# Optimization experiments

Hardware: AMD Instinct MI355X
Metric: run time of the kernel (lower is better)

Reference implementation:

```python
import jax, jax.numpy as jnp
import numpy as np

N_NODES = 100000
N_EDGES = 1600000
D_IN = 128
D_OUT = 128


def setup_inputs() -> dict:
    key = jax.random.key(0)
    k1, k2, k3, k4, k5, k6 = jax.random.split(key, 6)
    x = jax.random.normal(k1, (N_NODES, D_IN), dtype=jnp.float32)
    row = jnp.sort(jax.random.randint(k2, (N_EDGES,), 0, N_NODES, dtype=jnp.int32))
    col = jax.random.randint(k3, (N_EDGES,), 0, N_NODES, dtype=jnp.int32)
    val = jax.random.uniform(k4, (N_EDGES,), dtype=jnp.float32)
    # Glorot init for the two linear weights (stored as [in, out] for x @ W)
    std_l = float(np.sqrt(6.0 / (D_IN + D_OUT)))
    W_l = jax.random.uniform(k5, (D_IN, D_OUT), minval=-std_l, maxval=std_l, dtype=jnp.float32)
    b_l = jnp.zeros((D_OUT,), dtype=jnp.float32)
    W_r = jax.random.uniform(k6, (D_IN, D_OUT), minval=-std_l, maxval=std_l, dtype=jnp.float32)
    return {"x": x, "row": row, "col": col, "val": val, "W_l": W_l, "b_l": b_l, "W_r": W_r}


def reference(x, row, col, val, W_l, b_l, W_r):
    n = x.shape[0]
    # out_l = graph @ x  (sparse COO matmul: gather source feats, scale, scatter-add to rows)
    msg = val[:, None] * x[col]                      # [E, D_in]
    out_l = jax.ops.segment_sum(msg, row, num_segments=n)  # [N, D_in]
    # lin_l(out_l) + lin_r(x)
    return out_l @ W_l + b_l + x @ W_r
```

## Files before the change

### kernel.cpp

```cpp
#include <hip/hip_runtime.h>

#define D 128
#define EDGE_CAP 1024
typedef unsigned int uint32;
typedef __bf16 bf16x8 __attribute__((ext_vector_type(8)));
typedef float f32x4 __attribute__((ext_vector_type(4)));

__device__ __forceinline__ unsigned short f2bf(float f) {
    unsigned u = __float_as_uint(f);
    unsigned r = u + 0x7FFFu + ((u >> 16) & 1u);
    return (unsigned short)(r >> 16);
}
__device__ __forceinline__ float bflo(uint32 u) { return __uint_as_float(u << 16); }
__device__ __forceinline__ float bfhi(uint32 u) { return __uint_as_float(u & 0xFFFF0000u); }

__device__ __forceinline__ void fma8(float* acc, uint4 r, float v) {
    acc[0] += v * bflo(r.x); acc[1] += v * bfhi(r.x);
    acc[2] += v * bflo(r.y); acc[3] += v * bfhi(r.y);
    acc[4] += v * bflo(r.z); acc[5] += v * bfhi(r.z);
    acc[6] += v * bflo(r.w); acc[7] += v * bfhi(r.w);
}

__global__ __launch_bounds__(256) void prep_kernel(
    const float* __restrict__ x, unsigned short* __restrict__ xh, int n8,
    const int* __restrict__ row, int* __restrict__ row_ptr,
    int n_nodes, int n_edges,
    const float* __restrict__ Wl, const float* __restrict__ Wr,
    unsigned short* __restrict__ Wlt, unsigned short* __restrict__ Wrt,
    int nbConv, int nbRp) {
    const int b = blockIdx.x;
    if (b < nbConv) {
        const int id = b * 256 + threadIdx.x;
        if (id < n8) {
            const float4* p = (const float4*)x + (size_t)id * 2;
            float4 a = p[0], bb = p[1];
            uint4 o;
            o.x = f2bf(a.x) | ((uint32)f2bf(a.y) << 16);
            o.y = f2bf(a.z) | ((uint32)f2bf(a.w) << 16);
            o.z = f2bf(bb.x) | ((uint32)f2bf(bb.y) << 16);
            o.w = f2bf(bb.z) | ((uint32)f2bf(bb.w) << 16);
            ((uint4*)xh)[id] = o;
        }
    } else if (b < nbConv + nbRp) {
        const int e = (b - nbConv) * 256 + threadIdx.x;
        if (e < n_edges) {
            const int r = row[e];
            const int rp = (e == 0) ? -1 : row[e - 1];
            for (int n = rp + 1; n <= r; ++n) row_ptr[n] = e;
            if (e == n_edges - 1)
                for (int n = r + 1; n <= n_nodes; ++n) row_ptr[n] = n_edges;
        }
    } else {
        const int id = (b - nbConv - nbRp) * 256 + threadIdx.x;
        if (id < 16384) {
            const int n = id & 127, k = id >> 7;
            Wlt[n * 128 + k] = f2bf(Wl[k * 128 + n]);
            Wrt[n * 128 + k] = f2bf(Wr[k * 128 + n]);
        }
    }
}

__global__ __launch_bounds__(256) void spmm_gemm_kernel(
    const unsigned short* __restrict__ xh,
    const int* __restrict__ row_ptr,
    const int* __restrict__ col,
    const float* __restrict__ val,
    const unsigned short* __restrict__ Wlt,
    const unsigned short* __restrict__ Wrt,
    const float* __restrict__ b_l,
    float* __restrict__ out, int n_nodes) {
    __shared__ int2 scv[EDGE_CAP];
    __shared__ unsigned short A_lds[16][264];
    const int tid = threadIdx.x;
    const int n0 = blockIdx.x * 16;
    const int e0 = row_ptr[n0];
    const int e1 = row_ptr[min(n0 + 16, n_nodes)];
    const int ne = e1 - e0;
    const bool fits = (ne <= EDGE_CAP);
    if (fits) {
        for (int t = tid; t < ne; t += 256)
            scv[t] = make_int2(col[e0 + t], __float_as_int(val[e0 + t]));
    }

    {
        const int r = tid >> 4, ch = tid & 15;
        uint4 v = make_uint4(0u, 0u, 0u, 0u);
        if (n0 + r < n_nodes)
            v = *(const uint4*)&xh[(size_t)(n0 + r) * D + ch * 8];
        *(uint4*)&A_lds[r][128 + ch * 8] = v;
    }
    __syncthreads();

    const int wv = tid >> 6, lane = tid & 63;
    const int g = lane >> 4, lq = lane & 15;
    const int nloc = wv * 4 + g;
    const int n = n0 + nloc;

    int s = 0, e = 0;
    if (n < n_nodes) { s = row_ptr[n]; e = row_ptr[n + 1]; }

    float acc[8] = {0.f, 0.f, 0.f, 0.f, 0.f, 0.f, 0.f, 0.f};

    if (fits) {
        auto fetch = [&](int idx, int& c, float& v) {
            if (idx < e) {
                const int li = idx - e0;
                if (li < EDGE_CAP) { c = scv[li].x; v = __int_as_float(scv[li].y); }
                else               { c = col[idx]; v = val[idx]; }
            } else { c = 0; v = 0.f; }
        };

        int i = s;
        int c0, c1, c2, c3; float v0, v1, v2, v3;
        fetch(i + 0, c0, v0); fetch(i + 1, c1, v1);
        fetch(i + 2, c2, v2); fetch(i + 3, c3, v3);
        uint4 r0 = *(const uint4*)&xh[c0 * D + lq * 8];
        uint4 r1 = *(const uint4*)&xh[c1 * D + lq * 8];
        uint4 r2 = *(const uint4*)&xh[c2 * D + lq * 8];
        uint4 r3 = *(const uint4*)&xh[c3 * D + lq * 8];

        while (i < e) {
            const int i2 = i + 4;
            int d0, d1, d2, d3; float w0, w1, w2, w3;
            fetch(i2 + 0, d0, w0); fetch(i2 + 1, d1, w1);
            fetch(i2 + 2, d2, w2); fetch(i2 + 3, d3, w3);
            const uint4 t0 = *(const uint4*)&xh[d0 * D + lq * 8];
            const uint4 t1 = *(const uint4*)&xh[d1 * D + lq * 8];
            const uint4 t2 = *(const uint4*)&xh[d2 * D + lq * 8];
            const uint4 t3 = *(const uint4*)&xh[d3 * D + lq * 8];
            fma8(acc, r0, v0);
            fma8(acc, r1, v1);
            fma8(acc, r2, v2);
            fma8(acc, r3, v3);
            r0 = t0; r1 = t1; r2 = t2; r3 = t3;
            v0 = w0; v1 = w1; v2 = w2; v3 = w3;
            i = i2;
        }
    } else {
        for (int j = s; j < e; ++j) {
            const int c = col[j];
            const float v = val[j];
            const uint4 r = *(const uint4*)&xh[(size_t)c * D + lq * 8];
            fma8(acc, r, v);
        }
    }

    {
        uint4 o;
        o.x = f2bf(acc[0]) | ((uint32)f2bf(acc[1]) << 16);
        o.y = f2bf(acc[2]) | ((uint32)f2bf(acc[3]) << 16);
        o.z = f2bf(acc[4]) | ((uint32)f2bf(acc[5]) << 16);
        o.w = f2bf(acc[6]) | ((uint32)f2bf(acc[7]) << 16);
        *(uint4*)&A_lds[nloc][lq * 8] = o;
    }
    __syncthreads();

    const int fr = lane & 15;
    const int kofs = (lane >> 4) * 8;
    f32x4 acc2[2];
    acc2[0] = (f32x4){0.f, 0.f, 0.f, 0.f};
    acc2[1] = (f32x4){0.f, 0.f, 0.f, 0.f};
#pragma unroll
    for (int st = 0; st < 8; ++st) {
        const int k0 = st * 32;
        const unsigned short* Wsel = (k0 < 128) ? Wlt : Wrt;
        const int kk = k0 & 127;
        const bf16x8 a = *(const bf16x8*)&A_lds[fr][k0 + kofs];
#pragma unroll
        for (int nr = 0; nr < 2; ++nr) {
            const int ncol = wv * 32 + nr * 16 + fr;
            const bf16x8 b = *(const bf16x8*)&Wsel[ncol * 128 + kk + kofs];
            acc2[nr] = __builtin_amdgcn_mfma_f32_16x16x32_bf16(
                a, b, acc2[nr], 0, 0, 0);
        }
    }
    const int r0c = (lane >> 4) * 4;
#pragma unroll
    for (int nr = 0; nr < 2; ++nr) {
        const int ncol = wv * 32 + nr * 16 + fr;
        const float bias = b_l[ncol];
#pragma unroll
        for (int j = 0; j < 4; ++j) {
            const int m = n0 + r0c + j;
            if (m < n_nodes) out[(size_t)m * D + ncol] = acc2[nr][j] + bias;
        }
    }
}

__global__ void build_rowptr_kernel(const int* __restrict__ row,
                                    int* __restrict__ row_ptr,
                                    int n_nodes, int n_edges) {
    int e = blockIdx.x * blockDim.x + threadIdx.x;
    if (e >= n_edges) return;
    int r = row[e];
    int rp = (e == 0) ? -1 : row[e - 1];
    for (int n = rp + 1; n <= r; ++n) row_ptr[n] = e;
    if (e == n_edges - 1)
        for (int n = r + 1; n <= n_nodes; ++n) row_ptr[n] = n_edges;
}

__global__ __launch_bounds__(128) void spmm_kernel(
    const float* __restrict__ x, const int* __restrict__ row_ptr,
    const int* __restrict__ col, const float* __restrict__ val,
    float* __restrict__ out_l) {
    const int n = blockIdx.x;
    const int d = threadIdx.x;
    const int start = row_ptr[n];
    const int end = row_ptr[n + 1];
    float acc = 0.0f;
    for (int e = start; e < end; ++e)
        acc += val[e] * x[(size_t)col[e] * D + d];
    out_l[(size_t)n * D + d] = acc;
}

__global__ __launch_bounds__(256) void fused_gemm_kernel(
    const float* __restrict__ xin, const float* __restrict__ W_l,
    const float* __restrict__ b_l, const float* __restrict__ W_r,
    float* __restrict__ out, int M) {
    __shared__ float As[64][68];
    __shared__ float Ws[64][132];
    const int tid = threadIdx.x;
    const int tx = tid & 15;
    const int ty = tid >> 4;
    const int ty4 = ty * 4;
    const int m0 = blockIdx.x * 64;
    float acc[4][8];
#pragma unroll
    for (int i = 0; i < 4; ++i)
#pragma unroll
        for (int j = 0; j < 8; ++j) acc[i][j] = 0.0f;
    for (int kt = 0; kt < 4; ++kt) {
        const float* Asrc = (kt < 2) ? out : xin;
        const float* Wsrc = (kt < 2) ? W_l : W_r;
        const int koff = (kt & 1) * 64;
        __syncthreads();
#pragma unroll
        for (int r = 0; r < 4; ++r) {
            const int idx = tid + r * 256;
            const int m = idx >> 4;
            const int kq = idx & 15;
            float4 a = make_float4(0.f, 0.f, 0.f, 0.f);
            if (m0 + m < M)
                a = *(const float4*)&Asrc[(size_t)(m0 + m) * D + koff + kq * 4];
            *(float4*)&As[m][kq * 4] = a;
        }
#pragma unroll
        for (int r = 0; r < 8; ++r) {
            const int idx = tid + r * 256;
            const int k = idx >> 5;
            const int j4 = idx & 31;
            *(float4*)&Ws[k][j4 * 4] =
                *(const float4*)&Wsrc[(size_t)(koff + k) * D + j4 * 4];
        }
        __syncthreads();
#pragma unroll 4
        for (int k = 0; k < 64; ++k) {
            const float a0 = As[ty4 + 0][k], a1 = As[ty4 + 1][k];
            const float a2 = As[ty4 + 2][k], a3 = As[ty4 + 3][k];
            const float4 w0 = *(const float4*)&Ws[k][tx * 4];
            const float4 w1 = *(const float4*)&Ws[k][64 + tx * 4];
            acc[0][0] += a0 * w0.x; acc[0][1] += a0 * w0.y; acc[0][2] += a0 * w0.z; acc[0][3] += a0 * w0.w;
            acc[0][4] += a0 * w1.x; acc[0][5] += a0 * w1.y; acc[0][6] += a0 * w1.z; acc[0][7] += a0 * w1.w;
            acc[1][0] += a1 * w0.x; acc[1][1] += a1 * w0.y; acc[1][2] += a1 * w0.z; acc[1][3] += a1 * w0.w;
            acc[1][4] += a1 * w1.x; acc[1][5] += a1 * w1.y; acc[1][6] += a1 * w1.z; acc[1][7] += a1 * w1.w;
            acc[2][0] += a2 * w0.x; acc[2][1] += a2 * w0.y; acc[2][2] += a2 * w0.z; acc[2][3] += a2 * w0.w;
            acc[2][4] += a2 * w1.x; acc[2][5] += a2 * w1.y; acc[2][6] += a2 * w1.z; acc[2][7] += a2 * w1.w;
            acc[3][0] += a3 * w0.x; acc[3][1] += a3 * w0.y; acc[3][2] += a3 * w0.z; acc[3][3] += a3 * w0.w;
            acc[3][4] += a3 * w1.x; acc[3][5] += a3 * w1.y; acc[3][6] += a3 * w1.z; acc[3][7] += a3 * w1.w;
        }
    }
    const float4 bv0 = *(const float4*)&b_l[tx * 4];
    const float4 bv1 = *(const float4*)&b_l[64 + tx * 4];
#pragma unroll
    for (int i = 0; i < 4; ++i) {
        const int m = m0 + ty4 + i;
        if (m < M) {
            float4 o0, o1;
            o0.x = acc[i][0] + bv0.x; o0.y = acc[i][1] + bv0.y;
            o0.z = acc[i][2] + bv0.z; o0.w = acc[i][3] + bv0.w;
            o1.x = acc[i][4] + bv1.x; o1.y = acc[i][5] + bv1.y;
            o1.z = acc[i][6] + bv1.z; o1.w = acc[i][7] + bv1.w;
            *(float4*)&out[(size_t)m * D + tx * 4] = o0;
            *(float4*)&out[(size_t)m * D + 64 + tx * 4] = o1;
        }
    }
}

static inline size_t align256(size_t x) { return (x + 255) & ~(size_t)255; }

extern "C" void kernel_launch(void* const* d_in, const int* in_sizes, int n_in,
                              void* d_out, int out_size, void* d_ws, size_t ws_size,
                              hipStream_t stream) {
    const float* x   = (const float*)d_in[0];
    const int*   row = (const int*)d_in[1];
    const int*   col = (const int*)d_in[2];
    const float* val = (const float*)d_in[3];
    const float* W_l = (const float*)d_in[4];
    const float* b_l = (const float*)d_in[5];
    const float* W_r = (const float*)d_in[6];
    float* out = (float*)d_out;

    const int n_nodes = in_sizes[0] / D;
    const int n_edges = in_sizes[1];

    const size_t xh_bytes = (size_t)n_nodes * D * 2;
    const size_t wt_bytes = (size_t)D * D * 2;
    const size_t rp_bytes = (size_t)(n_nodes + 1) * 4;
    size_t off = 0;
    const size_t xh_off  = off; off += align256(xh_bytes);
    const size_t wlt_off = off; off += align256(wt_bytes);
    const size_t wrt_off = off; off += align256(wt_bytes);
    const size_t rp_off  = off; off += align256(rp_bytes);
    const size_t needed  = off + 65536;

    if (ws_size >= needed) {
        unsigned short* xh  = (unsigned short*)((char*)d_ws + xh_off);
        unsigned short* Wlt = (unsigned short*)((char*)d_ws + wlt_off);
        unsigned short* Wrt = (unsigned short*)((char*)d_ws + wrt_off);
        int* row_ptr        = (int*)((char*)d_ws + rp_off);

        const int n8 = n_nodes * D / 8;
        const int nbConv = (n8 + 255) / 256;
        const int nbRp   = (n_edges + 255) / 256;
        const int nbW    = 64;
        prep_kernel<<<nbConv + nbRp + nbW, 256, 0, stream>>>(
            x, xh, n8, row, row_ptr, n_nodes, n_edges,
            W_l, W_r, Wlt, Wrt, nbConv, nbRp);
        spmm_gemm_kernel<<<(n_nodes + 15) / 16, 256, 0, stream>>>(
            xh, row_ptr, col, val, Wlt, Wrt, b_l, out, n_nodes);
    } else {
        int* row_ptr = (int*)d_ws;
        build_rowptr_kernel<<<(n_edges + 255) / 256, 256, 0, stream>>>(
            row, row_ptr, n_nodes, n_edges);
        spmm_kernel<<<n_nodes, 128, 0, stream>>>(x, row_ptr, col, val, out);
        fused_gemm_kernel<<<(n_nodes + 63) / 64, 256, 0, stream>>>(
            x, W_l, b_l, W_r, out, n_nodes);
    }
}
```

Before: 108.9 us.

## Process 64 nodes per block with per-wave 16-row tiles and full-width MFMA

Each block now handles 64 nodes instead of 16, and each wave owns 16 rows end to end. A wave runs the SpMM for its rows (4 rows per lane group), writes them to a swizzled per-wave LDS tile, then computes all 128 output columns with MFMA, reading the x rows for the right-hand term straight from global memory. This drops the second block-wide barrier and cuts per-block overhead by a factor of four. In exchange there are fewer blocks, more serial SpMM work per lane group and larger edge staging (2048), which may lower occupancy and latency hiding.

Measured after the change: 140.8 us. +29.3%, slower.

```diff
diff --git a/kernel.cpp b/kernel.cpp
--- a/kernel.cpp
+++ b/kernel.cpp
@@ -1,7 +1,7 @@
 #include <hip/hip_runtime.h>
 
 #define D 128
-#define EDGE_CAP 1024
+#define ECAP 2048
 typedef unsigned int uint32;
 typedef __bf16 bf16x8 __attribute__((ext_vector_type(8)));
 typedef float f32x4 __attribute__((ext_vector_type(4)));
@@ -69,120 +69,123 @@
     const unsigned short* __restrict__ Wrt,
     const float* __restrict__ b_l,
     float* __restrict__ out, int n_nodes) {
-    __shared__ int2 scv[EDGE_CAP];
-    __shared__ unsigned short A_lds[16][264];
+    __shared__ int2 scv[ECAP];
+    __shared__ unsigned short A_w[4][16][128];
     const int tid = threadIdx.x;
-    const int n0 = blockIdx.x * 16;
-    const int e0 = row_ptr[n0];
-    const int e1 = row_ptr[min(n0 + 16, n_nodes)];
-    const int ne = e1 - e0;
-    const bool fits = (ne <= EDGE_CAP);
+    const int n0 = blockIdx.x * 64;
+    const int E0 = row_ptr[n0];
+    const int E1 = row_ptr[min(n0 + 64, n_nodes)];
+    const int ne = E1 - E0;
+    const bool fits = (ne <= ECAP);
     if (fits) {
         for (int t = tid; t < ne; t += 256)
-            scv[t] = make_int2(col[e0 + t], __float_as_int(val[e0 + t]));
-    }
-
-    {
-        const int r = tid >> 4, ch = tid & 15;
-        uint4 v = make_uint4(0u, 0u, 0u, 0u);
-        if (n0 + r < n_nodes)
-            v = *(const uint4*)&xh[(size_t)(n0 + r) * D + ch * 8];
-        *(uint4*)&A_lds[r][128 + ch * 8] = v;
+            scv[t] = make_int2(col[E0 + t], __float_as_int(val[E0 + t]));
     }
     __syncthreads();
 
     const int wv = tid >> 6, lane = tid & 63;
     const int g = lane >> 4, lq = lane & 15;
-    const int nloc = wv * 4 + g;
-    const int n = n0 + nloc;
-
-    int s = 0, e = 0;
-    if (n < n_nodes) { s = row_ptr[n]; e = row_ptr[n + 1]; }
-
-    float acc[8] = {0.f, 0.f, 0.f, 0.f, 0.f, 0.f, 0.f, 0.f};
-
-    if (fits) {
-        auto fetch = [&](int idx, int& c, float& v) {
-            if (idx < e) {
-                const int li = idx - e0;
-                if (li < EDGE_CAP) { c = scv[li].x; v = __int_as_float(scv[li].y); }
-                else               { c = col[idx]; v = val[idx]; }
-            } else { c = 0; v = 0.f; }
-        };
-
-        int i = s;
-        int c0, c1, c2, c3; float v0, v1, v2, v3;
-        fetch(i + 0, c0, v0); fetch(i + 1, c1, v1);
-        fetch(i + 2, c2, v2); fetch(i + 3, c3, v3);
-        uint4 r0 = *(const uint4*)&xh[c0 * D + lq * 8];
-        uint4 r1 = *(const uint4*)&xh[c1 * D + lq * 8];
-        uint4 r2 = *(const uint4*)&xh[c2 * D + lq * 8];
-        uint4 r3 = *(const uint4*)&xh[c3 * D + lq * 8];
-
-        while (i < e) {
-            const int i2 = i + 4;
-            int d0, d1, d2, d3; float w0, w1, w2, w3;
-            fetch(i2 + 0, d0, w0); fetch(i2 + 1, d1, w1);
-            fetch(i2 + 2, d2, w2); fetch(i2 + 3, d3, w3);
-            const uint4 t0 = *(const uint4*)&xh[d0 * D + lq * 8];
-            const uint4 t1 = *(const uint4*)&xh[d1 * D + lq * 8];
-            const uint4 t2 = *(const uint4*)&xh[d2 * D + lq * 8];
-            const uint4 t3 = *(const uint4*)&xh[d3 * D + lq * 8];
-            fma8(acc, r0, v0);
-            fma8(acc, r1, v1);
-            fma8(acc, r2, v2);
-            fma8(acc, r3, v3);
-            r0 = t0; r1 = t1; r2 = t2; r3 = t3;
-            v0 = w0; v1 = w1; v2 = w2; v3 = w3;
-            i = i2;
-        }
-    } else {
-        for (int j = s; j < e; ++j) {
-            const int c = col[j];
-            const float v = val[j];
-            const uint4 r = *(const uint4*)&xh[(size_t)c * D + lq * 8];
-            fma8(acc, r, v);
-        }
-    }
-
-    {
+    const int nw0 = n0 + wv * 16;
+
+    for (int i = 0; i < 4; ++i) {
+        const int rowl = g * 4 + i;
+        const int node = nw0 + rowl;
+        int s = 0, e = 0;
+        if (node < n_nodes) { s = row_ptr[node]; e = row_ptr[node + 1]; }
+
+        float acc[8] = {0.f, 0.f, 0.f, 0.f, 0.f, 0.f, 0.f, 0.f};
+
+        if (fits) {
+            auto fetch = [&](int idx, int& c, float& v) {
+                if (idx < e) {
+                    const int li = idx - E0;
+                    c = scv[li].x; v = __int_as_float(scv[li].y);
+                } else { c = 0; v = 0.f; }
+            };
+            int ii = s;
+            int c0, c1, c2, c3; float v0, v1, v2, v3;
+            fetch(ii + 0, c0, v0); fetch(ii + 1, c1, v1);
+            fetch(ii + 2, c2, v2); fetch(ii + 3, c3, v3);
+            uint4 r0 = *(const uint4*)&xh[c0 * D + lq * 8];
+            uint4 r1 = *(const uint4*)&xh[c1 * D + lq * 8];
+            uint4 r2 = *(const uint4*)&xh[c2 * D + lq * 8];
+            uint4 r3 = *(const uint4*)&xh[c3 * D + lq * 8];
+            while (ii < e) {
+                const int i2 = ii + 4;
+                int d0, d1, d2, d3; float w0, w1, w2, w3;
+                fetch(i2 + 0, d0, w0); fetch(i2 + 1, d1, w1);
+                fetch(i2 + 2, d2, w2); fetch(i2 + 3, d3, w3);
+                const uint4 t0 = *(const uint4*)&xh[d0 * D + lq * 8];
+                const uint4 t1 = *(const uint4*)&xh[d1 * D + lq * 8];
+                const uint4 t2 = *(const uint4*)&xh[d2 * D + lq * 8];
+                const uint4 t3 = *(const uint4*)&xh[d3 * D + lq * 8];
+                fma8(acc, r0, v0);
+                fma8(acc, r1, v1);
+                fma8(acc, r2, v2);
+                fma8(acc, r3, v3);
+                r0 = t0; r1 = t1; r2 = t2; r3 = t3;
+                v0 = w0; v1 = w1; v2 = w2; v3 = w3;
+                ii = i2;
+            }
+        } else {
+            for (int j = s; j < e; ++j) {
+                const int c = col[j];
+                const float v = val[j];
+                const uint4 r = *(const uint4*)&xh[(size_t)c * D + lq * 8];
+                fma8(acc, r, v);
+            }
+        }
+
         uint4 o;
         o.x = f2bf(acc[0]) | ((uint32)f2bf(acc[1]) << 16);
         o.y = f2bf(acc[2]) | ((uint32)f2bf(acc[3]) << 16);
         o.z = f2bf(acc[4]) | ((uint32)f2bf(acc[5]) << 16);
         o.w = f2bf(acc[6]) | ((uint32)f2bf(acc[7]) << 16);
-        *(uint4*)&A_lds[nloc][lq * 8] = o;
-    }
-    __syncthreads();
-
-    const int fr = lane & 15;
-    const int kofs = (lane >> 4) * 8;
-    f32x4 acc2[2];
-    acc2[0] = (f32x4){0.f, 0.f, 0.f, 0.f};
-    acc2[1] = (f32x4){0.f, 0.f, 0.f, 0.f};
-#pragma unroll
-    for (int st = 0; st < 8; ++st) {
+        const int sidx = (lq * 8) ^ ((rowl & 7) << 3);
+        *(uint4*)&A_w[wv][rowl][sidx] = o;
+    }
+
+    const int fr = lane & 15, hh = lane >> 4;
+    const int kofs = hh * 8;
+    f32x4 acc2[8];
+#pragma unroll
+    for (int nt = 0; nt < 8; ++nt) acc2[nt] = (f32x4){0.f, 0.f, 0.f, 0.f};
+
+#pragma unroll
+    for (int st = 0; st < 4; ++st) {
         const int k0 = st * 32;
-        const unsigned short* Wsel = (k0 < 128) ? Wlt : Wrt;
-        const int kk = k0 & 127;
-        const bf16x8 a = *(const bf16x8*)&A_lds[fr][k0 + kofs];
-#pragma unroll
-        for (int nr = 0; nr < 2; ++nr) {
-            const int ncol = wv * 32 + nr * 16 + fr;
-            const bf16x8 b = *(const bf16x8*)&Wsel[ncol * 128 + kk + kofs];
-            acc2[nr] = __builtin_amdgcn_mfma_f32_16x16x32_bf16(
-                a, b, acc2[nr], 0, 0, 0);
-        }
-    }
-    const int r0c = (lane >> 4) * 4;
-#pragma unroll
-    for (int nr = 0; nr < 2; ++nr) {
-        const int ncol = wv * 32 + nr * 16 + fr;
+        const int aidx = (k0 + kofs) ^ ((fr & 7) << 3);
+        const bf16x8 a = *(const bf16x8*)&A_w[wv][fr][aidx];
+#pragma unroll
+        for (int nt = 0; nt < 8; ++nt) {
+            const bf16x8 b =
+                *(const bf16x8*)&Wlt[(nt * 16 + fr) * 128 + k0 + kofs];
+            acc2[nt] = __builtin_amdgcn_mfma_f32_16x16x32_bf16(
+                a, b, acc2[nt], 0, 0, 0);
+        }
+    }
+#pragma unroll
+    for (int st = 0; st < 4; ++st) {
+        const int k0 = st * 32;
+        const bf16x8 a =
+            *(const bf16x8*)&xh[(size_t)(nw0 + fr) * D + k0 + kofs];
+#pragma unroll
+        for (int nt = 0; nt < 8; ++nt) {
+            const bf16x8 b =
+                *(const bf16x8*)&Wrt[(nt * 16 + fr) * 128 + k0 + kofs];
+            acc2[nt] = __builtin_amdgcn_mfma_f32_16x16x32_bf16(
+                a, b, acc2[nt], 0, 0, 0);
+        }
+    }
+
+#pragma unroll
+    for (int nt = 0; nt < 8; ++nt) {
+        const int ncol = nt * 16 + fr;
         const float bias = b_l[ncol];
 #pragma unroll
         for (int j = 0; j < 4; ++j) {
-            const int m = n0 + r0c + j;
-            if (m < n_nodes) out[(size_t)m * D + ncol] = acc2[nr][j] + bias;
+            const int m = nw0 + hh * 4 + j;
+            if (m < n_nodes) out[(size_t)m * D + ncol] = acc2[nt][j] + bias;
         }
     }
 }
@@ -326,7 +329,7 @@
         prep_kernel<<<nbConv + nbRp + nbW, 256, 0, stream>>>(
             x, xh, n8, row, row_ptr, n_nodes, n_edges,
             W_l, W_r, Wlt, Wrt, nbConv, nbRp);
-        spmm_gemm_kernel<<<(n_nodes + 15) / 16, 256, 0, stream>>>(
+        spmm_gemm_kernel<<<(n_nodes + 63) / 64, 256, 0, stream>>>(
             xh, row_ptr, col, val, Wlt, Wrt, b_l, out, n_nodes);
     } else {
         int* row_ptr = (int*)d_ws;
```

## Process two 16-node tiles per block, overlapping staging with MFMA epilogue

Applied to the files above, without the earlier changes.

Each block now handles 32 nodes as two 16-row tiles with double-buffered LDS. The edge list and x rows for the second tile are staged while the first tile's MFMA epilogue runs, aiming to hide load latency and amortize W loads. LDS rows are XOR-swizzled instead of padded to avoid bank conflicts. The grid is halved, which reduces the number of blocks available for parallelism, and the in-loop fallback to global memory for edges beyond the LDS cap was removed.

Result: slower. 125.2 us (+15.0%).

```diff
diff --git a/kernel.cpp b/kernel.cpp
--- a/kernel.cpp
+++ b/kernel.cpp
@@ -70,120 +70,140 @@
     const float* __restrict__ b_l,
     float* __restrict__ out, int n_nodes) {
     __shared__ int2 scv[EDGE_CAP];
-    __shared__ unsigned short A_lds[16][264];
+    __shared__ unsigned short A[2][16][256];
     const int tid = threadIdx.x;
-    const int n0 = blockIdx.x * 16;
-    const int e0 = row_ptr[n0];
-    const int e1 = row_ptr[min(n0 + 16, n_nodes)];
-    const int ne = e1 - e0;
-    const bool fits = (ne <= EDGE_CAP);
-    if (fits) {
-        for (int t = tid; t < ne; t += 256)
-            scv[t] = make_int2(col[e0 + t], __float_as_int(val[e0 + t]));
-    }
-
-    {
-        const int r = tid >> 4, ch = tid & 15;
+    const int wv = tid >> 6, lane = tid & 63;
+    const int g = lane >> 4, lq = lane & 15;
+
+    const int n0a = blockIdx.x * 32;
+    const int n0b = n0a + 16;
+    const bool haveB = (n0b < n_nodes);
+
+    int e0a = 0, e0b = 0;
+    bool fita = false, fitb = false;
+
+    auto stage_scv = [&](int n0, int& e0, bool& fits) {
+        e0 = row_ptr[n0];
+        const int e1 = row_ptr[min(n0 + 16, n_nodes)];
+        const int ne = e1 - e0;
+        fits = (ne <= EDGE_CAP);
+        if (fits) {
+            for (int t = tid; t < ne; t += 256)
+                scv[t] = make_int2(col[e0 + t], __float_as_int(val[e0 + t]));
+        }
+    };
+    auto stage_x = [&](int buf, int n0) {
+        const int r = tid >> 4, c = tid & 15;
         uint4 v = make_uint4(0u, 0u, 0u, 0u);
         if (n0 + r < n_nodes)
-            v = *(const uint4*)&xh[(size_t)(n0 + r) * D + ch * 8];
-        *(uint4*)&A_lds[r][128 + ch * 8] = v;
-    }
-    __syncthreads();
-
-    const int wv = tid >> 6, lane = tid & 63;
-    const int g = lane >> 4, lq = lane & 15;
-    const int nloc = wv * 4 + g;
-    const int n = n0 + nloc;
-
-    int s = 0, e = 0;
-    if (n < n_nodes) { s = row_ptr[n]; e = row_ptr[n + 1]; }
-
-    float acc[8] = {0.f, 0.f, 0.f, 0.f, 0.f, 0.f, 0.f, 0.f};
-
-    if (fits) {
-        auto fetch = [&](int idx, int& c, float& v) {
-            if (idx < e) {
-                const int li = idx - e0;
-                if (li < EDGE_CAP) { c = scv[li].x; v = __int_as_float(scv[li].y); }
-                else               { c = col[idx]; v = val[idx]; }
-            } else { c = 0; v = 0.f; }
-        };
-
-        int i = s;
-        int c0, c1, c2, c3; float v0, v1, v2, v3;
-        fetch(i + 0, c0, v0); fetch(i + 1, c1, v1);
-        fetch(i + 2, c2, v2); fetch(i + 3, c3, v3);
-        uint4 r0 = *(const uint4*)&xh[c0 * D + lq * 8];
-        uint4 r1 = *(const uint4*)&xh[c1 * D + lq * 8];
-        uint4 r2 = *(const uint4*)&xh[c2 * D + lq * 8];
-        uint4 r3 = *(const uint4*)&xh[c3 * D + lq * 8];
-
-        while (i < e) {
-            const int i2 = i + 4;
-            int d0, d1, d2, d3; float w0, w1, w2, w3;
-            fetch(i2 + 0, d0, w0); fetch(i2 + 1, d1, w1);
-            fetch(i2 + 2, d2, w2); fetch(i2 + 3, d3, w3);
-            const uint4 t0 = *(const uint4*)&xh[d0 * D + lq * 8];
-            const uint4 t1 = *(const uint4*)&xh[d1 * D + lq * 8];
-            const uint4 t2 = *(const uint4*)&xh[d2 * D + lq * 8];
-            const uint4 t3 = *(const uint4*)&xh[d3 * D + lq * 8];
-            fma8(acc, r0, v0);
-            fma8(acc, r1, v1);
-            fma8(acc, r2, v2);
-            fma8(acc, r3, v3);
-            r0 = t0; r1 = t1; r2 = t2; r3 = t3;
-            v0 = w0; v1 = w1; v2 = w2; v3 = w3;
-            i = i2;
-        }
-    } else {
-        for (int j = s; j < e; ++j) {
-            const int c = col[j];
-            const float v = val[j];
-            const uint4 r = *(const uint4*)&xh[(size_t)c * D + lq * 8];
-            fma8(acc, r, v);
-        }
-    }
-
-    {
+            v = *(const uint4*)&xh[(size_t)(n0 + r) * D + c * 8];
+        *(uint4*)&A[buf][r][128 + ((c ^ (r & 7)) * 8)] = v;
+    };
+
+    auto gather = [&](int buf, int n0, int e0, bool fits) {
+        const int nloc = wv * 4 + g;
+        const int n = n0 + nloc;
+        int s = 0, e = 0;
+        if (n < n_nodes) { s = row_ptr[n]; e = row_ptr[n + 1]; }
+        float acc[8] = {0.f, 0.f, 0.f, 0.f, 0.f, 0.f, 0.f, 0.f};
+
+        if (fits) {
+            auto fetch = [&](int idx, int& c, float& v) {
+                if (idx < e) {
+                    const int li = idx - e0;
+                    c = scv[li].x; v = __int_as_float(scv[li].y);
+                } else { c = 0; v = 0.f; }
+            };
+            int i = s;
+            int c0, c1, c2, c3; float v0, v1, v2, v3;
+            fetch(i + 0, c0, v0); fetch(i + 1, c1, v1);
+            fetch(i + 2, c2, v2); fetch(i + 3, c3, v3);
+            uint4 r0 = *(const uint4*)&xh[c0 * D + lq * 8];
+            uint4 r1 = *(const uint4*)&xh[c1 * D + lq * 8];
+            uint4 r2 = *(const uint4*)&xh[c2 * D + lq * 8];
+            uint4 r3 = *(const uint4*)&xh[c3 * D + lq * 8];
+            while (i < e) {
+                const int i2 = i + 4;
+                int d0, d1, d2, d3; float w0, w1, w2, w3;
+                fetch(i2 + 0, d0, w0); fetch(i2 + 1, d1, w1);
+                fetch(i2 + 2, d2, w2); fetch(i2 + 3, d3, w3);
+                const uint4 t0 = *(const uint4*)&xh[d0 * D + lq * 8];
+                const uint4 t1 = *(const uint4*)&xh[d1 * D + lq * 8];
+                const uint4 t2 = *(const uint4*)&xh[d2 * D + lq * 8];
+                const uint4 t3 = *(const uint4*)&xh[d3 * D + lq * 8];
+                fma8(acc, r0, v0);
+                fma8(acc, r1, v1);
+                fma8(acc, r2, v2);
+                fma8(acc, r3, v3);
+                r0 = t0; r1 = t1; r2 = t2; r3 = t3;
+                v0 = w0; v1 = w1; v2 = w2; v3 = w3;
+                i = i2;
+            }
+        } else {
+            for (int j = s; j < e; ++j) {
+                const int c = col[j];
+                const float v = val[j];
+                const uint4 r = *(const uint4*)&xh[(size_t)c * D + lq * 8];
+                fma8(acc, r, v);
+            }
+        }
+
         uint4 o;
         o.x = f2bf(acc[0]) | ((uint32)f2bf(acc[1]) << 16);
         o.y = f2bf(acc[2]) | ((uint32)f2bf(acc[3]) << 16);
         o.z = f2bf(acc[4]) | ((uint32)f2bf(acc[5]) << 16);
         o.w = f2bf(acc[6]) | ((uint32)f2bf(acc[7]) << 16);
-        *(uint4*)&A_lds[nloc][lq * 8] = o;
-    }
-    __syncthreads();
-
-    const int fr = lane & 15;
-    const int kofs = (lane >> 4) * 8;
-    f32x4 acc2[2];
-    acc2[0] = (f32x4){0.f, 0.f, 0.f, 0.f};
-    acc2[1] = (f32x4){0.f, 0.f, 0.f, 0.f};
-#pragma unroll
-    for (int st = 0; st < 8; ++st) {
-        const int k0 = st * 32;
-        const unsigned short* Wsel = (k0 < 128) ? Wlt : Wrt;
-        const int kk = k0 & 127;
-        const bf16x8 a = *(const bf16x8*)&A_lds[fr][k0 + kofs];
+        *(uint4*)&A[buf][nloc][(lq ^ (nloc & 7)) * 8] = o;
+    };
+
+    auto epilogue = [&](int buf, int n0) {
+        const int fr = lane & 15, hh = lane >> 4;
+        const int kofs = hh * 8;
+        f32x4 acc2[2];
+        acc2[0] = (f32x4){0.f, 0.f, 0.f, 0.f};
+        acc2[1] = (f32x4){0.f, 0.f, 0.f, 0.f};
+#pragma unroll
+        for (int st = 0; st < 8; ++st) {
+            const int h = st >> 2;
+            const int cc = (st & 3) * 4 + hh;
+            const bf16x8 a =
+                *(const bf16x8*)&A[buf][fr][h * 128 + ((cc ^ (fr & 7)) * 8)];
+            const unsigned short* Wsel = h ? Wrt : Wlt;
+            const int kk = (st & 3) * 32 + kofs;
+#pragma unroll
+            for (int nr = 0; nr < 2; ++nr) {
+                const int ncol = wv * 32 + nr * 16 + fr;
+                const bf16x8 b = *(const bf16x8*)&Wsel[ncol * 128 + kk];
+                acc2[nr] = __builtin_amdgcn_mfma_f32_16x16x32_bf16(
+                    a, b, acc2[nr], 0, 0, 0);
+            }
+        }
+        const int r0c = hh * 4;
 #pragma unroll
         for (int nr = 0; nr < 2; ++nr) {
             const int ncol = wv * 32 + nr * 16 + fr;
-            const bf16x8 b = *(const bf16x8*)&Wsel[ncol * 128 + kk + kofs];
-            acc2[nr] = __builtin_amdgcn_mfma_f32_16x16x32_bf16(
-                a, b, acc2[nr], 0, 0, 0);
-        }
-    }
-    const int r0c = (lane >> 4) * 4;
-#pragma unroll
-    for (int nr = 0; nr < 2; ++nr) {
-        const int ncol = wv * 32 + nr * 16 + fr;
-        const float bias = b_l[ncol];
-#pragma unroll
-        for (int j = 0; j < 4; ++j) {
-            const int m = n0 + r0c + j;
-            if (m < n_nodes) out[(size_t)m * D + ncol] = acc2[nr][j] + bias;
-        }
+            const float bias = b_l[ncol];
+#pragma unroll
+            for (int j = 0; j < 4; ++j) {
+                const int m = n0 + r0c + j;
+                if (m < n_nodes)
+                    out[(size_t)m * D + ncol] = acc2[nr][j] + bias;
+            }
+        }
+    };
+
+    stage_scv(n0a, e0a, fita);
+    stage_x(0, n0a);
+    __syncthreads();
+    gather(0, n0a, e0a, fita);
+    __syncthreads();
+    if (haveB) { stage_scv(n0b, e0b, fitb); stage_x(1, n0b); }
+    epilogue(0, n0a);
+    __syncthreads();
+    if (haveB) {
+        gather(1, n0b, e0b, fitb);
+        __syncthreads();
+        epilogue(1, n0b);
     }
 }
 
@@ -326,7 +346,7 @@
         prep_kernel<<<nbConv + nbRp + nbW, 256, 0, stream>>>(
             x, xh, n8, row, row_ptr, n_nodes, n_edges,
             W_l, W_r, Wlt, Wrt, nbConv, nbRp);
-        spmm_gemm_kernel<<<(n_nodes + 15) / 16, 256, 0, stream>>>(
+        spmm_gemm_kernel<<<(n_nodes + 31) / 32, 256, 0, stream>>>(
             xh, row_ptr, col, val, Wlt, Wrt, b_l, out, n_nodes);
     } else {
         int* row_ptr = (int*)d_ws;
```

## Balance SpMM edges evenly across row groups with shared-memory atomic accumulation

Applied to the files above, without the earlier changes.

Each 16-lane group now takes an equal slice of the block's edges instead of one row's edges. The local row index is packed into the high bits of the cached column value. Partial sums are flushed into a float shared-memory accumulator with LDS atomics whenever the row changes. This removes load imbalance from rows with very different degrees, at the cost of LDS atomics, an extra 8KB of shared memory, a zeroing pass and reading the row array.

Measured after the change: 168.0 us. 54.3% more time.

```diff
diff --git a/kernel.cpp b/kernel.cpp
--- a/kernel.cpp
+++ b/kernel.cpp
@@ -63,6 +63,7 @@
 __global__ __launch_bounds__(256) void spmm_gemm_kernel(
     const unsigned short* __restrict__ xh,
     const int* __restrict__ row_ptr,
+    const int* __restrict__ row,
     const int* __restrict__ col,
     const float* __restrict__ val,
     const unsigned short* __restrict__ Wlt,
@@ -70,18 +71,28 @@
     const float* __restrict__ b_l,
     float* __restrict__ out, int n_nodes) {
     __shared__ int2 scv[EDGE_CAP];
+    __shared__ float Aacc[16][128];
     __shared__ unsigned short A_lds[16][264];
     const int tid = threadIdx.x;
     const int n0 = blockIdx.x * 16;
-    const int e0 = row_ptr[n0];
-    const int e1 = row_ptr[min(n0 + 16, n_nodes)];
-    const int ne = e1 - e0;
+    const int E0 = row_ptr[n0];
+    const int E1 = row_ptr[min(n0 + 16, n_nodes)];
+    const int ne = E1 - E0;
     const bool fits = (ne <= EDGE_CAP);
+
+    {
+        const int r = tid >> 4, ch = tid & 15;
+        const float4 z = make_float4(0.f, 0.f, 0.f, 0.f);
+        *(float4*)&Aacc[r][ch * 8] = z;
+        *(float4*)&Aacc[r][ch * 8 + 4] = z;
+    }
     if (fits) {
-        for (int t = tid; t < ne; t += 256)
-            scv[t] = make_int2(col[e0 + t], __float_as_int(val[e0 + t]));
-    }
-
+        for (int t = tid; t < ne; t += 256) {
+            const int rl = row[E0 + t] - n0;
+            scv[t] = make_int2(col[E0 + t] | (rl << 24),
+                               __float_as_int(val[E0 + t]));
+        }
+    }
     {
         const int r = tid >> 4, ch = tid & 15;
         uint4 v = make_uint4(0u, 0u, 0u, 0u);
@@ -93,65 +104,97 @@
 
     const int wv = tid >> 6, lane = tid & 63;
     const int g = lane >> 4, lq = lane & 15;
-    const int nloc = wv * 4 + g;
-    const int n = n0 + nloc;
-
-    int s = 0, e = 0;
-    if (n < n_nodes) { s = row_ptr[n]; e = row_ptr[n + 1]; }
-
-    float acc[8] = {0.f, 0.f, 0.f, 0.f, 0.f, 0.f, 0.f, 0.f};
+    const int gb = wv * 4 + g;
 
     if (fits) {
-        auto fetch = [&](int idx, int& c, float& v) {
-            if (idx < e) {
-                const int li = idx - e0;
-                if (li < EDGE_CAP) { c = scv[li].x; v = __int_as_float(scv[li].y); }
-                else               { c = col[idx]; v = val[idx]; }
-            } else { c = 0; v = 0.f; }
+        const int chunk = (ne + 15) >> 4;
+        const int cs = gb * chunk;
+        const int ce = min(cs + chunk, ne);
+
+        float acc[8] = {0.f, 0.f, 0.f, 0.f, 0.f, 0.f, 0.f, 0.f};
+        int rcur = -1;
+
+        auto fetchq = [&](int li, int& c, float& v, int& rl) {
+            if (li < ce) {
+                const int2 p = scv[li];
+                c = p.x & 0x00FFFFFF;
+                rl = (p.x >> 24) & 0xF;
+                v = __int_as_float(p.y);
+            } else { c = 0; v = 0.f; rl = -1; }
         };
-
-        int i = s;
-        int c0, c1, c2, c3; float v0, v1, v2, v3;
-        fetch(i + 0, c0, v0); fetch(i + 1, c1, v1);
-        fetch(i + 2, c2, v2); fetch(i + 3, c3, v3);
-        uint4 r0 = *(const uint4*)&xh[c0 * D + lq * 8];
-        uint4 r1 = *(const uint4*)&xh[c1 * D + lq * 8];
-        uint4 r2 = *(const uint4*)&xh[c2 * D + lq * 8];
-        uint4 r3 = *(const uint4*)&xh[c3 * D + lq * 8];
-
-        while (i < e) {
+        auto flush = [&]() {
+            if (rcur >= 0) {
+#pragma unroll
+                for (int jj = 0; jj < 8; ++jj) {
+                    atomicAdd(&Aacc[rcur][lq * 8 + jj], acc[jj]);
+                    acc[jj] = 0.f;
+                }
+            }
+        };
+        auto consume = [&](uint4 rd, float v, int rl) {
+            if (rl >= 0) {
+                if (rl != rcur) { flush(); rcur = rl; }
+                fma8(acc, rd, v);
+            }
+        };
+
+        int i = cs;
+        int c0, c1, c2, c3, l0, l1, l2, l3; float v0, v1, v2, v3;
+        fetchq(i + 0, c0, v0, l0); fetchq(i + 1, c1, v1, l1);
+        fetchq(i + 2, c2, v2, l2); fetchq(i + 3, c3, v3, l3);
+        uint4 d0 = *(const uint4*)&xh[c0 * D + lq * 8];
+        uint4 d1 = *(const uint4*)&xh[c1 * D + lq * 8];
+        uint4 d2 = *(const uint4*)&xh[c2 * D + lq * 8];
+        uint4 d3 = *(const uint4*)&xh[c3 * D + lq * 8];
+
+        while (i < ce) {
             const int i2 = i + 4;
-            int d0, d1, d2, d3; float w0, w1, w2, w3;
-            fetch(i2 + 0, d0, w0); fetch(i2 + 1, d1, w1);
-            fetch(i2 + 2, d2, w2); fetch(i2 + 3, d3, w3);
-            const uint4 t0 = *(const uint4*)&xh[d0 * D + lq * 8];
-            const uint4 t1 = *(const uint4*)&xh[d1 * D + lq * 8];
-            const uint4 t2 = *(const uint4*)&xh[d2 * D + lq * 8];
-            const uint4 t3 = *(const uint4*)&xh[d3 * D + lq * 8];
-            fma8(acc, r0, v0);
-            fma8(acc, r1, v1);
-            fma8(acc, r2, v2);
-            fma8(acc, r3, v3);
-            r0 = t0; r1 = t1; r2 = t2; r3 = t3;
+            int e0_, e1_, e2_, e3_, s0_, s1_, s2_, s3_;
+            float w0, w1, w2, w3;
+            fetchq(i2 + 0, e0_, w0, s0_); fetchq(i2 + 1, e1_, w1, s1_);
+            fetchq(i2 + 2, e2_, w2, s2_); fetchq(i2 + 3, e3_, w3, s3_);
+            const uint4 t0 = *(const uint4*)&xh[e0_ * D + lq * 8];
+            const uint4 t1 = *(const uint4*)&xh[e1_ * D + lq * 8];
+            const uint4 t2 = *(const uint4*)&xh[e2_ * D + lq * 8];
+            const uint4 t3 = *(const uint4*)&xh[e3_ * D + lq * 8];
+            consume(d0, v0, l0);
+            consume(d1, v1, l1);
+            consume(d2, v2, l2);
+            consume(d3, v3, l3);
+            d0 = t0; d1 = t1; d2 = t2; d3 = t3;
             v0 = w0; v1 = w1; v2 = w2; v3 = w3;
+            l0 = s0_; l1 = s1_; l2 = s2_; l3 = s3_;
             i = i2;
         }
+        flush();
     } else {
-        for (int j = s; j < e; ++j) {
-            const int c = col[j];
-            const float v = val[j];
-            const uint4 r = *(const uint4*)&xh[(size_t)c * D + lq * 8];
-            fma8(acc, r, v);
-        }
-    }
+        const int n = n0 + gb;
+        if (n < n_nodes) {
+            const int s = row_ptr[n], e = row_ptr[n + 1];
+            float acc[8] = {0.f, 0.f, 0.f, 0.f, 0.f, 0.f, 0.f, 0.f};
+            for (int j = s; j < e; ++j) {
+                const int c = col[j];
+                const float v = val[j];
+                const uint4 r = *(const uint4*)&xh[(size_t)c * D + lq * 8];
+                fma8(acc, r, v);
+            }
+#pragma unroll
+            for (int jj = 0; jj < 8; ++jj)
+                Aacc[gb][lq * 8 + jj] = acc[jj];
+        }
+    }
+    __syncthreads();
 
     {
+        const int r = tid >> 4, ch = tid & 15;
+        const float4 a = *(const float4*)&Aacc[r][ch * 8];
+        const float4 b = *(const float4*)&Aacc[r][ch * 8 + 4];
         uint4 o;
-        o.x = f2bf(acc[0]) | ((uint32)f2bf(acc[1]) << 16);
-        o.y = f2bf(acc[2]) | ((uint32)f2bf(acc[3]) << 16);
-        o.z = f2bf(acc[4]) | ((uint32)f2bf(acc[5]) << 16);
-        o.w = f2bf(acc[6]) | ((uint32)f2bf(acc[7]) << 16);
-        *(uint4*)&A_lds[nloc][lq * 8] = o;
+        o.x = f2bf(a.x) | ((uint32)f2bf(a.y) << 16);
+        o.y = f2bf(a.z) | ((uint32)f2bf(a.w) << 16);
+        o.z = f2bf(b.x) | ((uint32)f2bf(b.y) << 16);
+        o.w = f2bf(b.z) | ((uint32)f2bf(b.w) << 16);
+        *(uint4*)&A_lds[r][ch * 8] = o;
     }
     __syncthreads();
 
@@ -313,7 +356,7 @@
     const size_t rp_off  = off; off += align256(rp_bytes);
     const size_t needed  = off + 65536;
 
-    if (ws_size >= needed) {
+    if (ws_size >= needed && n_nodes < (1 << 24)) {
         unsigned short* xh  = (unsigned short*)((char*)d_ws + xh_off);
         unsigned short* Wlt = (unsigned short*)((char*)d_ws + wlt_off);
         unsigned short* Wrt = (unsigned short*)((char*)d_ws + wrt_off);
@@ -327,7 +370,7 @@
             x, xh, n8, row, row_ptr, n_nodes, n_edges,
             W_l, W_r, Wlt, Wrt, nbConv, nbRp);
         spmm_gemm_kernel<<<(n_nodes + 15) / 16, 256, 0, stream>>>(
-            xh, row_ptr, col, val, Wlt, Wrt, b_l, out, n_nodes);
+            xh, row_ptr, row, col, val, Wlt, Wrt, b_l, out, n_nodes);
     } else {
         int* row_ptr = (int*)d_ws;
         build_rowptr_kernel<<<(n_edges + 255) / 256, 256, 0, stream>>>(
```
